# Kernel optimization log

Measured on AMD Instinct MI355X. Metric: run time of the kernel, lower is better.

The kernel has to match this reference:

```python
import jax, jax.numpy as jnp
import numpy as np

B, S, HID = 16, 577, 768
H, D = 12, 64          # heads, head_dim
N_KEEP = 576           # kept channels after structured pruning


def setup_inputs() -> dict:
    key = jax.random.key(0)
    ks = jax.random.split(key, 10)
    hs = jax.random.normal(ks[0], (B, S, HID), dtype=jnp.float32)
    Wq = jax.random.normal(ks[1], (HID, N_KEEP), dtype=jnp.float32) * 0.02
    bq = jax.random.normal(ks[2], (N_KEEP,), dtype=jnp.float32) * 0.02
    Wk = jax.random.normal(ks[3], (HID, N_KEEP), dtype=jnp.float32) * 0.02
    bk = jax.random.normal(ks[4], (N_KEEP,), dtype=jnp.float32) * 0.02
    Wv = jax.random.normal(ks[5], (HID, N_KEEP), dtype=jnp.float32) * 0.02
    bv = jax.random.normal(ks[6], (N_KEEP,), dtype=jnp.float32) * 0.02
    # positions of nonzero entries of the boolean padding masks (unique, sorted)
    q_idx = jnp.sort(jax.random.permutation(ks[7], HID)[:N_KEEP]).astype(jnp.int32)
    k_idx = jnp.sort(jax.random.permutation(ks[8], HID)[:N_KEEP]).astype(jnp.int32)
    v_idx = jnp.sort(jax.random.permutation(ks[9], HID)[:N_KEEP]).astype(jnp.int32)
    return {"hidden_states": hs, "Wq": Wq, "bq": bq, "Wk": Wk, "bk": bk,
            "Wv": Wv, "bv": bv, "q_idx": q_idx, "k_idx": k_idx, "v_idx": v_idx}


def _pad_and_split_heads(x, idx):
    # scatter pruned channels [B,S,N_KEEP] back into full layout [B,S,HID],
    # then split into heads -> [B,H,S,D]
    padded = jnp.zeros((B, S, HID), dtype=x.dtype).at[:, :, idx].set(x)
    return padded.reshape(B, S, H, D).transpose(0, 2, 1, 3)


def reference(hidden_states, Wq, bq, Wk, bk, Wv, bv, q_idx, k_idx, v_idx):
    q = hidden_states @ Wq + bq            # [B,S,N_KEEP]
    k = hidden_states @ Wk + bk
    v = hidden_states @ Wv + bv
    ql = _pad_and_split_heads(q, q_idx)     # [B,H,S,D]
    kl = _pad_and_split_heads(k, k_idx)
    vl = _pad_and_split_heads(v, v_idx)
    scale = 1.0 / np.float32(np.sqrt(D))
    scores = jnp.einsum('bhqd,bhkd->bhqk', ql, kl) * scale  # [B,H,S,S]
    probs = jax.nn.softmax(scores, axis=-1)
    ctx = jnp.einsum('bhqk,bhkd->bhqd', probs, vl)          # [B,H,S,D]
    ctx = ctx.transpose(0, 2, 1, 3).reshape(B, S, HID)       # [B,S,HID]
    return ctx[:, :, v_idx]                                  # gather kept channels
```

## Files before the change

kernel.cpp:

```cpp
#include <hip/hip_runtime.h>
#include <hip/hip_bf16.h>
#include <cstdint>
#include <cstddef>

#define B_     16
#define S_     577
#define HID_   768
#define H_     12
#define D_     64
#define NKEEP_ 576
#define MROWS  (B_ * S_)
#define BHROWS (B_ * H_ * S_)
#define N4     (MROWS * HID_ / 4)

typedef __bf16 bf16;
typedef __bf16 bf16x8 __attribute__((ext_vector_type(8)));
typedef float  f32x4  __attribute__((ext_vector_type(4)));

__device__ __forceinline__ void gload16(const bf16* g, bf16* l) {
    __builtin_amdgcn_global_load_lds(
        (const __attribute__((address_space(1))) unsigned int*)g,
        (__attribute__((address_space(3))) unsigned int*)l, 16, 0, 0);
}

__device__ __forceinline__ float fexp2(float x) {
#if __has_builtin(__builtin_amdgcn_exp2f)
    return __builtin_amdgcn_exp2f(x);
#else
    return exp2f(x);
#endif
}

#define WAITBAR(N) asm volatile("s_waitcnt vmcnt(" #N ") lgkmcnt(0)\n\ts_barrier" ::: "memory")

__global__ __launch_bounds__(256) void k_prep(const float* __restrict__ hs,
                                              const float* __restrict__ Wq,
                                              const float* __restrict__ Wk,
                                              const float* __restrict__ Wv,
                                              const float* __restrict__ bq,
                                              const float* __restrict__ bk,
                                              const float* __restrict__ bv,
                                              const int* __restrict__ qi,
                                              const int* __restrict__ ki,
                                              const int* __restrict__ vi,
                                              bf16* __restrict__ hs_bf,
                                              bf16* __restrict__ Wp_t,
                                              int* __restrict__ inv,
                                              float* __restrict__ bias_p) {
    __shared__ float tile[64][33];
    const int bid = blockIdx.x, t = threadIdx.x;
    if (bid < 54) {
        const int p = bid / 18;
        const int j0 = (bid % 18) * 32;
        const float* W  = (p == 0) ? Wq : (p == 1) ? Wk : Wv;
        const int* idx  = (p == 0) ? qi : (p == 1) ? ki : vi;
        bf16* dst = Wp_t + (size_t)p * HID_ * HID_;
        const int lj = t & 31, lk = t >> 5;
        const int sj = t >> 3, ke = (t & 7) * 8;
        const int c = idx[j0 + sj];
        for (int kt = 0; kt < HID_; kt += 64) {
            __syncthreads();
#pragma unroll
            for (int i = 0; i < 8; ++i)
                tile[lk + i * 8][lj] = W[(size_t)(kt + lk + i * 8) * NKEEP_ + j0 + lj];
            __syncthreads();
            union { bf16 h[8]; bf16x8 v; } o;
#pragma unroll
            for (int i = 0; i < 8; ++i) o.h[i] = (bf16)tile[ke + i][sj];
            *reinterpret_cast<bf16x8*>(dst + (size_t)c * HID_ + kt + ke) = o.v;
        }
    } else if (bid == 54) {
        for (int i = t; i < 3 * HID_; i += 256) { inv[i] = -1; bias_p[i] = 0.0f; }
        __syncthreads();
        for (int i = t; i < 3 * NKEEP_; i += 256) {
            const int p = i / NKEEP_, j = i % NKEEP_;
            const int* src = (p == 0) ? qi : (p == 1) ? ki : vi;
            const float* bb = (p == 0) ? bq : (p == 1) ? bk : bv;
            const int c = src[j];
            inv[p * HID_ + c] = j;
            bias_p[p * HID_ + c] = bb[j];
        }
    } else {
        const int i = (bid - 55) * 256 + t;
        if (i < N4) {
            float4 v = reinterpret_cast<const float4*>(hs)[i];
            union { bf16 h[4]; uint2 u; } o;
            o.h[0] = (bf16)v.x; o.h[1] = (bf16)v.y;
            o.h[2] = (bf16)v.z; o.h[3] = (bf16)v.w;
            reinterpret_cast<uint2*>(hs_bf)[i] = o.u;
        }
    }
}

#define BM 128
#define BN 256
#define BK 32
#define NT 24
#define BUFE 12288

__global__ __launch_bounds__(256, 2) void k_gemm(const bf16* __restrict__ X,
                                                 const bf16* __restrict__ Wp_t,
                                                 const float* __restrict__ bias_p,
                                                 bf16* __restrict__ Qo, bf16* __restrict__ Ko,
                                                 bf16* __restrict__ Vo) {
    __shared__ bf16 smem[3 * BUFE];

    const int xcd = blockIdx.x & 7, pos = blockIdx.x >> 3;
    const int L = xcd * 82 + (xcd > 0 ? 1 : 0) + pos;
    const int m0 = (L / 9) * BM;
    const int np = L % 9;
    const int n0 = (np % 3) * BN;
    const int p  = np / 3;

    const bf16* Wbase = Wp_t + (size_t)p * HID_ * HID_;
    bf16* Obase = (p == 0) ? Qo : (p == 1) ? Ko : Vo;
    const float osc = (p == 0) ? 0.125f * 1.44269504f : 1.0f;

    const int t = threadIdx.x;
    const int wid = t >> 6, lane = t & 63;
    const int wr = wid >> 1, wc = wid & 1;
    const int lrow = lane & 15, g = lane >> 4, lk = (lane >> 4) * 8;
    const int srow = lane >> 2, scol = (lane & 3) * 8;

    const bf16* Xs = X + (size_t)m0 * HID_;
    const bf16* Ws = Wbase + (size_t)n0 * HID_;

    f32x4 acc[4][8] = {};

#define STAGE(buf, kk)                                                          \
    {                                                                           \
        _Pragma("unroll")                                                       \
        for (int i_ = 0; i_ < 2; ++i_) {                                        \
            const int c_ = wid * 2 + i_;                                        \
            gload16(Xs + (size_t)(c_ * 16 + srow) * HID_ + (kk) + scol,         \
                    smem + (buf) * BUFE + c_ * 512);                            \
        }                                                                       \
        _Pragma("unroll")                                                       \
        for (int i_ = 0; i_ < 4; ++i_) {                                        \
            const int c_ = wid * 4 + i_;                                        \
            gload16(Ws + (size_t)(c_ * 16 + srow) * HID_ + (kk) + scol,         \
                    smem + (buf) * BUFE + 4096 + c_ * 512);                     \
        }                                                                       \
    }

#define COMPUTE(buf)                                                            \
    {                                                                           \
        const bf16* As_ = smem + (buf) * BUFE;                                  \
        const bf16* Bs_ = As_ + 4096;                                           \
        bf16x8 af[4], bfr[8];                                                   \
        _Pragma("unroll")                                                       \
        for (int m = 0; m < 4; ++m)                                             \
            af[m] = *reinterpret_cast<const bf16x8*>(                           \
                &As_[(wr * 64 + m * 16 + lrow) * BK + lk]);                     \
        _Pragma("unroll")                                                       \
        for (int n = 0; n < 8; ++n)                                             \
            bfr[n] = *reinterpret_cast<const bf16x8*>(                          \
                &Bs_[(wc * 128 + n * 16 + lrow) * BK + lk]);                    \
        _Pragma("unroll")                                                       \
        for (int m = 0; m < 4; ++m)                                             \
            _Pragma("unroll")                                                   \
            for (int n = 0; n < 8; ++n)                                         \
                acc[m][n] = __builtin_amdgcn_mfma_f32_16x16x32_bf16(            \
                    af[m], bfr[n], acc[m][n], 0, 0, 0);                         \
    }

    STAGE(0, 0)
    STAGE(1, BK)
    WAITBAR(6);

    int kk_next = 2 * BK;
    for (int u = 0; u < 7; ++u) {
#pragma unroll
        for (int j = 0; j < 3; ++j) {
            STAGE((j + 2) % 3, kk_next)
            COMPUTE(j)
            WAITBAR(6);
            kk_next += BK;
        }
    }
    STAGE(2, 23 * BK)
    COMPUTE(0)
    WAITBAR(6);
    COMPUTE(1)
    WAITBAR(0);
    COMPUTE(2)
#undef STAGE
#undef COMPUTE

    float bias_n[8];
#pragma unroll
    for (int n = 0; n < 8; ++n)
        bias_n[n] = bias_p[p * HID_ + n0 + wc * 128 + n * 16 + lrow];

    const int rowl = t >> 2, cq = t & 3;
#pragma unroll
    for (int half = 0; half < 2; ++half) {
        __syncthreads();
        if (wr == half) {
#pragma unroll
            for (int n = 0; n < 8; ++n)
#pragma unroll
                for (int m = 0; m < 4; ++m)
#pragma unroll
                    for (int r = 0; r < 4; ++r)
                        smem[(m * 16 + g * 4 + r) * 260 + wc * 128 + n * 16 + lrow] =
                            (bf16)((acc[m][n][r] + bias_n[n]) * osc);
        }
        __syncthreads();
        const int grow = m0 + half * 64 + rowl;
        if (grow < MROWS) {
            const int b = grow / S_, s = grow % S_;
            const size_t rbase = ((size_t)b * H_ * S_ + s) * D_;
#pragma unroll
            for (int i = 0; i < 8; ++i) {
                const int c0 = i * 32 + cq * 8;
                bf16x8 v = *reinterpret_cast<const bf16x8*>(&smem[rowl * 260 + c0]);
                const int c = n0 + c0, h = c >> 6, d = c & 63;
                *reinterpret_cast<bf16x8*>(&Obase[rbase + (size_t)h * S_ * D_ + d]) = v;
            }
        }
    }
}

#define KB2  64
#define VLD2 72
#define KVSZ (KB2 * VLD2)

__global__ __launch_bounds__(512, 4) void k_attn(const bf16* __restrict__ Q,
                                                 const bf16* __restrict__ K,
                                                 const bf16* __restrict__ V,
                                                 const int* __restrict__ inv,
                                                 float* __restrict__ out) {
    __shared__ bf16 Ksm[2][KVSZ];
    __shared__ bf16 Vsm[2][KVSZ];

    const int bid = blockIdx.x;
    const int bh = bid % (B_ * H_);
    const int q0 = (bid / (B_ * H_)) * 128;
    const int t = threadIdx.x, wid = t >> 6, lane = t & 63;
    const int lcol = lane & 15, g = lane >> 4;

    const bf16* Qb = Q + (size_t)bh * S_ * D_;
    const bf16* Kb = K + (size_t)bh * S_ * D_;
    const bf16* Vb = V + (size_t)bh * S_ * D_;

    const int qrow = q0 + wid * 16 + lcol;
    bf16x8 qf0 = {}, qf1 = {};
    if (qrow < S_) {
        qf0 = *reinterpret_cast<const bf16x8*>(Qb + (size_t)qrow * D_ + g * 8);
        qf1 = *reinterpret_cast<const bf16x8*>(Qb + (size_t)qrow * D_ + 32 + g * 8);
    }

    const int key_t = t >> 3;
    const int a_t = t & 7;
    const int ch_t = a_t * 8;
    const int ks_s = key_t >> 4, g_s = (key_t >> 2) & 3, r_s = key_t & 3;
    const int pos = (ks_s >> 1) * 32 + g_s * 8 + (ks_s & 1) * 4 + r_s;

    float lrun = 0.f;
    f32x4 oT[4] = {};
    const bf16x8 zv = {};

    bf16x8 kreg = zv, vreg = zv;
    if (key_t < S_) {
        kreg = *reinterpret_cast<const bf16x8*>(Kb + (size_t)key_t * D_ + ch_t);
        vreg = *reinterpret_cast<const bf16x8*>(Vb + (size_t)key_t * D_ + ch_t);
    }

    int cur = 0;
    for (int k0 = 0; k0 < S_; k0 += KB2) {
        *reinterpret_cast<bf16x8*>(&Ksm[cur][key_t * VLD2 + ch_t]) = kreg;
#pragma unroll
        for (int i = 0; i < 8; ++i) {
            int ch = (pos >> 3) ^ i ^ a_t;
            Vsm[cur][(ch_t + i) * VLD2 + ch * 8 + (pos & 7)] = vreg[i];
        }
        __syncthreads();

        if (k0 + KB2 < S_) {
            int gk = k0 + KB2 + key_t;
            if (gk < S_) {
                kreg = *reinterpret_cast<const bf16x8*>(Kb + (size_t)gk * D_ + ch_t);
                vreg = *reinterpret_cast<const bf16x8*>(Vb + (size_t)gk * D_ + ch_t);
            } else { kreg = zv; vreg = zv; }
        }

        f32x4 sv[4];
        __builtin_amdgcn_s_setprio(1);
#pragma unroll
        for (int ks = 0; ks < 4; ++ks) {
            const bf16* kr = &Ksm[cur][(ks * 16 + lcol) * VLD2];
            bf16x8 kf0 = *reinterpret_cast<const bf16x8*>(kr + g * 8);
            bf16x8 kf1 = *reinterpret_cast<const bf16x8*>(kr + 32 + g * 8);
            f32x4 z = {};
            z = __builtin_amdgcn_mfma_f32_16x16x32_bf16(kf0, qf0, z, 0, 0, 0);
            z = __builtin_amdgcn_mfma_f32_16x16x32_bf16(kf1, qf1, z, 0, 0, 0);
            sv[ks] = z;
        }
        __builtin_amdgcn_s_setprio(0);
        if (k0 + KB2 > S_) {
#pragma unroll
            for (int ks = 0; ks < 4; ++ks)
#pragma unroll
                for (int r = 0; r < 4; ++r)
                    if (k0 + ks * 16 + g * 4 + r >= S_) sv[ks][r] = -INFINITY;
        }

        union { bf16 h[16]; bf16x8 v[2]; } pu;
        float rs = 0.f;
#pragma unroll
        for (int ks = 0; ks < 4; ++ks)
#pragma unroll
            for (int r = 0; r < 4; ++r) {
                float pv = fexp2(sv[ks][r]);
                rs += pv;
                pu.h[ks * 4 + r] = (bf16)pv;
            }
        lrun += rs;

        __builtin_amdgcn_s_setprio(1);
#pragma unroll
        for (int kh = 0; kh < 2; ++kh) {
#pragma unroll
            for (int tt = 0; tt < 4; ++tt) {
                int d = tt * 16 + lcol;
                int s3 = (d ^ (d >> 3)) & 7;
                int ch = (kh * 4 + g) ^ s3;
                bf16x8 vf = *reinterpret_cast<const bf16x8*>(&Vsm[cur][d * VLD2 + ch * 8]);
                oT[tt] = __builtin_amdgcn_mfma_f32_16x16x32_bf16(vf, pu.v[kh], oT[tt], 0, 0, 0);
            }
        }
        __builtin_amdgcn_s_setprio(0);
        cur ^= 1;
    }

    lrun += __shfl_xor(lrun, 16);
    lrun += __shfl_xor(lrun, 32);

    if (qrow < S_) {
        const int b = bh / H_, h = bh % H_;
        const int* invv = inv + 2 * HID_;
        float invl = 1.0f / lrun;
        float* orow = out + ((size_t)b * S_ + qrow) * NKEEP_;
#pragma unroll
        for (int tt = 0; tt < 4; ++tt)
#pragma unroll
            for (int r = 0; r < 4; ++r) {
                int d = tt * 16 + g * 4 + r;
                int j = invv[h * D_ + d];
                if (j >= 0) orow[j] = oT[tt][r] * invl;
            }
    }
}

extern "C" void kernel_launch(void* const* d_in, const int* in_sizes, int n_in,
                              void* d_out, int out_size, void* d_ws, size_t ws_size,
                              hipStream_t stream) {
    const float* hs = (const float*)d_in[0];
    const float* Wq = (const float*)d_in[1];
    const float* bq = (const float*)d_in[2];
    const float* Wk = (const float*)d_in[3];
    const float* bk = (const float*)d_in[4];
    const float* Wv = (const float*)d_in[5];
    const float* bv = (const float*)d_in[6];
    const int* qi = (const int*)d_in[7];
    const int* ki = (const int*)d_in[8];
    const int* vi = (const int*)d_in[9];
    float* out = (float*)d_out;

    char* ws = (char*)d_ws;
    size_t off = 0;
    bf16* hs_bf = (bf16*)(ws + off); off += (size_t)MROWS * HID_ * 2;
    bf16* Wp_t  = (bf16*)(ws + off); off += (size_t)3 * HID_ * HID_ * 2;
    float* bias_p = (float*)(ws + off); off += 3 * HID_ * 4;
    int* inv = (int*)(ws + off); off += 3 * HID_ * 4;
    bf16* Qw = (bf16*)(ws + off); off += (size_t)BHROWS * D_ * 2;
    bf16* Kw = (bf16*)(ws + off); off += (size_t)BHROWS * D_ * 2;
    bf16* Vw = (bf16*)(ws + off); off += (size_t)BHROWS * D_ * 2;

    hipMemsetAsync(Wp_t, 0, (size_t)3 * HID_ * HID_ * 2, stream);
    const int nprep = 55 + (N4 + 255) / 256;
    k_prep<<<nprep, 256, 0, stream>>>(hs, Wq, Wk, Wv, bq, bk, bv, qi, ki, vi,
                                      hs_bf, Wp_t, inv, bias_p);
    k_gemm<<<657, 256, 0, stream>>>(hs_bf, Wp_t, bias_p, Qw, Kw, Vw);
    k_attn<<<5 * B_ * H_, 512, 0, stream>>>(Qw, Kw, Vw, inv, out);
}
```

Before: 108.9 us.

## Pad sequence to 584 and emit V pre-transposed from the projection GEMM

The QKV projection GEMM now writes V in a transposed [channel, padded-token] layout, and Q/K use a per-head sequence length padded to 584. The attention kernel can then store V tiles into LDS with plain vector writes, replacing the per-element swizzled transpose, and read V fragments with two 8-byte LDS loads. Padding also removes the bounds checks on Q, K and V loads. In exchange the GEMM epilogue for V does a strided LDS gather and strided global stores. The last tile reads past each head or batch into neighbouring data or uninitialised padding, which depends on the score masking and on that memory holding finite values.

```diff
diff --git a/kernel.cpp b/kernel.cpp
--- a/kernel.cpp
+++ b/kernel.cpp
@@ -5,13 +5,13 @@
 
 #define B_     16
 #define S_     577
+#define SP_    584
 #define HID_   768
 #define H_     12
 #define D_     64
 #define NKEEP_ 576
-#define MROWS  (B_ * S_)
-#define BHROWS (B_ * H_ * S_)
-#define N4     (MROWS * HID_ / 4)
+#define MP_    (B_ * SP_)
+#define NP4    (MP_ * HID_ / 4)
 
 typedef __bf16 bf16;
 typedef __bf16 bf16x8 __attribute__((ext_vector_type(8)));
@@ -82,12 +82,20 @@
         }
     } else {
         const int i = (bid - 55) * 256 + t;
-        if (i < N4) {
-            float4 v = reinterpret_cast<const float4*>(hs)[i];
-            union { bf16 h[4]; uint2 u; } o;
-            o.h[0] = (bf16)v.x; o.h[1] = (bf16)v.y;
-            o.h[2] = (bf16)v.z; o.h[3] = (bf16)v.w;
-            reinterpret_cast<uint2*>(hs_bf)[i] = o.u;
+        if (i < NP4) {
+            const int row = i / 192;
+            const int col = i - row * 192;
+            const int b = row / SP_;
+            const int s = row - b * SP_;
+            uint2 ov = {0u, 0u};
+            if (s < S_) {
+                float4 v = reinterpret_cast<const float4*>(hs)[((size_t)(b * S_ + s)) * 192 + col];
+                union { bf16 h[4]; uint2 u; } o;
+                o.h[0] = (bf16)v.x; o.h[1] = (bf16)v.y;
+                o.h[2] = (bf16)v.z; o.h[3] = (bf16)v.w;
+                ov = o.u;
+            }
+            reinterpret_cast<uint2*>(hs_bf)[(size_t)row * 192 + col] = ov;
         }
     }
 }
@@ -95,14 +103,13 @@
 #define BM 128
 #define BN 256
 #define BK 32
-#define NT 24
 #define BUFE 12288
 
 __global__ __launch_bounds__(256, 2) void k_gemm(const bf16* __restrict__ X,
                                                  const bf16* __restrict__ Wp_t,
                                                  const float* __restrict__ bias_p,
                                                  bf16* __restrict__ Qo, bf16* __restrict__ Ko,
-                                                 bf16* __restrict__ Vo) {
+                                                 bf16* __restrict__ Vt) {
     __shared__ bf16 smem[3 * BUFE];
 
     const int xcd = blockIdx.x & 7, pos = blockIdx.x >> 3;
@@ -113,7 +120,6 @@
     const int p  = np / 3;
 
     const bf16* Wbase = Wp_t + (size_t)p * HID_ * HID_;
-    bf16* Obase = (p == 0) ? Qo : (p == 1) ? Ko : Vo;
     const float osc = (p == 0) ? 0.125f * 1.44269504f : 1.0f;
 
     const int t = threadIdx.x;
@@ -207,16 +213,35 @@
                             (bf16)((acc[m][n][r] + bias_n[n]) * osc);
         }
         __syncthreads();
-        const int grow = m0 + half * 64 + rowl;
-        if (grow < MROWS) {
-            const int b = grow / S_, s = grow % S_;
-            const size_t rbase = ((size_t)b * H_ * S_ + s) * D_;
+        const int grow0 = m0 + half * 64;
+        if (p < 2) {
+            bf16* Obase = (p == 0) ? Qo : Ko;
+            const int grow = grow0 + rowl;
+            const int b = grow / SP_, s = grow - b * SP_;
+            const size_t rbase = ((size_t)(b * H_ + 0) * SP_) * D_;
+#pragma unroll
+            for (int i = 0; i < 4; ++i) {
+                const int c0 = i * 64 + cq * 8;
+                (void)rbase; (void)c0;
+            }
 #pragma unroll
             for (int i = 0; i < 8; ++i) {
                 const int c0 = i * 32 + cq * 8;
                 bf16x8 v = *reinterpret_cast<const bf16x8*>(&smem[rowl * 260 + c0]);
                 const int c = n0 + c0, h = c >> 6, d = c & 63;
-                *reinterpret_cast<bf16x8*>(&Obase[rbase + (size_t)h * S_ * D_ + d]) = v;
+                *reinterpret_cast<bf16x8*>(
+                    &Obase[(((size_t)(b * H_ + h) * SP_) + s) * D_ + d]) = v;
+            }
+        } else {
+            const int crow = n0 + t;
+            bf16* vrow = Vt + (size_t)crow * MP_;
+#pragma unroll
+            for (int rg = 0; rg < 8; ++rg) {
+                union { bf16 h8[8]; bf16x8 v; } pk;
+#pragma unroll
+                for (int i = 0; i < 8; ++i)
+                    pk.h8[i] = smem[(rg * 8 + i) * 260 + t];
+                *reinterpret_cast<bf16x8*>(&vrow[grow0 + rg * 8]) = pk.v;
             }
         }
     }
@@ -228,7 +253,7 @@
 
 __global__ __launch_bounds__(512, 4) void k_attn(const bf16* __restrict__ Q,
                                                  const bf16* __restrict__ K,
-                                                 const bf16* __restrict__ V,
+                                                 const bf16* __restrict__ Vt,
                                                  const int* __restrict__ inv,
                                                  float* __restrict__ out) {
     __shared__ bf16 Ksm[2][KVSZ];
@@ -239,50 +264,35 @@
     const int q0 = (bid / (B_ * H_)) * 128;
     const int t = threadIdx.x, wid = t >> 6, lane = t & 63;
     const int lcol = lane & 15, g = lane >> 4;
-
-    const bf16* Qb = Q + (size_t)bh * S_ * D_;
-    const bf16* Kb = K + (size_t)bh * S_ * D_;
-    const bf16* Vb = V + (size_t)bh * S_ * D_;
+    const int b = bh / H_, h = bh % H_;
+
+    const bf16* Qb = Q + (size_t)bh * SP_ * D_;
+    const bf16* Kb = K + (size_t)bh * SP_ * D_;
 
     const int qrow = q0 + wid * 16 + lcol;
-    bf16x8 qf0 = {}, qf1 = {};
-    if (qrow < S_) {
-        qf0 = *reinterpret_cast<const bf16x8*>(Qb + (size_t)qrow * D_ + g * 8);
-        qf1 = *reinterpret_cast<const bf16x8*>(Qb + (size_t)qrow * D_ + 32 + g * 8);
-    }
+    bf16x8 qf0 = *reinterpret_cast<const bf16x8*>(Qb + (size_t)qrow * D_ + g * 8);
+    bf16x8 qf1 = *reinterpret_cast<const bf16x8*>(Qb + (size_t)qrow * D_ + 32 + g * 8);
 
     const int key_t = t >> 3;
     const int a_t = t & 7;
     const int ch_t = a_t * 8;
-    const int ks_s = key_t >> 4, g_s = (key_t >> 2) & 3, r_s = key_t & 3;
-    const int pos = (ks_s >> 1) * 32 + g_s * 8 + (ks_s & 1) * 4 + r_s;
+    const bf16* Vrow = Vt + (size_t)(h * D_ + key_t) * MP_ + (size_t)b * SP_;
 
     float lrun = 0.f;
     f32x4 oT[4] = {};
-    const bf16x8 zv = {};
-
-    bf16x8 kreg = zv, vreg = zv;
-    if (key_t < S_) {
-        kreg = *reinterpret_cast<const bf16x8*>(Kb + (size_t)key_t * D_ + ch_t);
-        vreg = *reinterpret_cast<const bf16x8*>(Vb + (size_t)key_t * D_ + ch_t);
-    }
+
+    bf16x8 kreg = *reinterpret_cast<const bf16x8*>(Kb + (size_t)key_t * D_ + ch_t);
+    bf16x8 vreg = *reinterpret_cast<const bf16x8*>(Vrow + ch_t);
 
     int cur = 0;
     for (int k0 = 0; k0 < S_; k0 += KB2) {
         *reinterpret_cast<bf16x8*>(&Ksm[cur][key_t * VLD2 + ch_t]) = kreg;
-#pragma unroll
-        for (int i = 0; i < 8; ++i) {
-            int ch = (pos >> 3) ^ i ^ a_t;
-            Vsm[cur][(ch_t + i) * VLD2 + ch * 8 + (pos & 7)] = vreg[i];
-        }
+        *reinterpret_cast<bf16x8*>(&Vsm[cur][key_t * VLD2 + ch_t]) = vreg;
         __syncthreads();
 
         if (k0 + KB2 < S_) {
-            int gk = k0 + KB2 + key_t;
-            if (gk < S_) {
-                kreg = *reinterpret_cast<const bf16x8*>(Kb + (size_t)gk * D_ + ch_t);
-                vreg = *reinterpret_cast<const bf16x8*>(Vb + (size_t)gk * D_ + ch_t);
-            } else { kreg = zv; vreg = zv; }
+            kreg = *reinterpret_cast<const bf16x8*>(Kb + (size_t)(k0 + KB2 + key_t) * D_ + ch_t);
+            vreg = *reinterpret_cast<const bf16x8*>(Vrow + k0 + KB2 + ch_t);
         }
 
         f32x4 sv[4];
@@ -323,11 +333,12 @@
         for (int kh = 0; kh < 2; ++kh) {
 #pragma unroll
             for (int tt = 0; tt < 4; ++tt) {
-                int d = tt * 16 + lcol;
-                int s3 = (d ^ (d >> 3)) & 7;
-                int ch = (kh * 4 + g) ^ s3;
-                bf16x8 vf = *reinterpret_cast<const bf16x8*>(&Vsm[cur][d * VLD2 + ch * 8]);
-                oT[tt] = __builtin_amdgcn_mfma_f32_16x16x32_bf16(vf, pu.v[kh], oT[tt], 0, 0, 0);
+                const int d = tt * 16 + lcol;
+                const bf16* vr = &Vsm[cur][d * VLD2 + kh * 32 + 4 * g];
+                union { uint2 u[2]; bf16x8 v8; } vf;
+                vf.u[0] = *reinterpret_cast<const uint2*>(vr);
+                vf.u[1] = *reinterpret_cast<const uint2*>(vr + 16);
+                oT[tt] = __builtin_amdgcn_mfma_f32_16x16x32_bf16(vf.v8, pu.v[kh], oT[tt], 0, 0, 0);
             }
         }
         __builtin_amdgcn_s_setprio(0);
@@ -338,7 +349,6 @@
     lrun += __shfl_xor(lrun, 32);
 
     if (qrow < S_) {
-        const int b = bh / H_, h = bh % H_;
         const int* invv = inv + 2 * HID_;
         float invl = 1.0f / lrun;
         float* orow = out + ((size_t)b * S_ + qrow) * NKEEP_;
@@ -370,18 +380,19 @@
 
     char* ws = (char*)d_ws;
     size_t off = 0;
-    bf16* hs_bf = (bf16*)(ws + off); off += (size_t)MROWS * HID_ * 2;
+    const size_t PAD = 8192;
+    bf16* hs_bf = (bf16*)(ws + off); off += (size_t)MP_ * HID_ * 2 + PAD;
     bf16* Wp_t  = (bf16*)(ws + off); off += (size_t)3 * HID_ * HID_ * 2;
     float* bias_p = (float*)(ws + off); off += 3 * HID_ * 4;
     int* inv = (int*)(ws + off); off += 3 * HID_ * 4;
-    bf16* Qw = (bf16*)(ws + off); off += (size_t)BHROWS * D_ * 2;
-    bf16* Kw = (bf16*)(ws + off); off += (size_t)BHROWS * D_ * 2;
-    bf16* Vw = (bf16*)(ws + off); off += (size_t)BHROWS * D_ * 2;
+    bf16* Qw = (bf16*)(ws + off); off += (size_t)B_ * H_ * SP_ * D_ * 2 + PAD;
+    bf16* Kw = (bf16*)(ws + off); off += (size_t)B_ * H_ * SP_ * D_ * 2 + PAD;
+    bf16* Vt = (bf16*)(ws + off); off += (size_t)HID_ * MP_ * 2 + PAD;
 
     hipMemsetAsync(Wp_t, 0, (size_t)3 * HID_ * HID_ * 2, stream);
-    const int nprep = 55 + (N4 + 255) / 256;
+    const int nprep = 55 + (NP4 + 255) / 256;
     k_prep<<<nprep, 256, 0, stream>>>(hs, Wq, Wk, Wv, bq, bk, bv, qi, ki, vi,
                                       hs_bf, Wp_t, inv, bias_p);
-    k_gemm<<<657, 256, 0, stream>>>(hs_bf, Wp_t, bias_p, Qw, Kw, Vw);
-    k_attn<<<5 * B_ * H_, 512, 0, stream>>>(Qw, Kw, Vw, inv, out);
-}
+    k_gemm<<<657, 256, 0, stream>>>(hs_bf, Wp_t, bias_p, Qw, Kw, Vt);
+    k_attn<<<5 * B_ * H_, 512, 0, stream>>>(Qw, Kw, Vt, inv, out);
+}
```

After: 109.6 us. No clear change (+0.7%).
